# Kernel tuning notes

Hardware: AMD Instinct MI355X
Metric: run time of the kernel (lower is better)

The kernel has to match this reference:

```python
import jax, jax.numpy as jnp
import numpy as np

B, D, T = 32, 6, 2048
FH, ENC, H, CONF, NC, K = 128, 128, 256, 64, 10, 5


def setup_inputs() -> dict:
    key = jax.random.key(0)
    ks = iter(jax.random.split(key, 40))
    n = lambda shape, s=0.05: jax.random.normal(next(ks), shape, dtype=jnp.float32) * s
    inp = {
        'M': jax.random.normal(next(ks), (B, D, T), dtype=jnp.float32),
        # causal conv frontend (4 dilated convs, kernel 5)
        'conv_w0': n((FH, D, K)), 'conv_b0': n((FH,)),
        'conv_w1': n((FH, FH, K)), 'conv_b1': n((FH,)),
        'conv_w2': n((FH, FH, K)), 'conv_b2': n((FH,)),
        'conv_w3': n((FH, FH, K)), 'conv_b3': n((FH,)),
        # encoder projection
        'enc_w': n((ENC, FH)), 'enc_b': n((ENC,)),
        # selective state space
        'A': n((H, H), 0.01), 'ip_w': n((H, ENC)), 'ip_b': n((H,)),
        'state_bias': jnp.zeros((H,), jnp.float32),
        'op_w': n((H, H)), 'op_b': n((H,)),
        # classifier head
        'cls_w1': n((256, H)), 'cls_b1': n((256,)),
        'cls_w2': n((NC, 256)), 'cls_b2': n((NC,)),
        # metanet: 2*D -> 64 -> 128 -> confound_dim
        'mn_w1': n((64, 2 * D)), 'mn_b1': n((64,)),
        'mn_w2': n((128, 64)), 'mn_b2': n((128,)),
        'mn_w3': n((CONF, 128)), 'mn_b3': n((CONF,)),
        # frontdoor: confound_dim -> 128 -> ssm_hidden
        'fd_w1': n((128, CONF)), 'fd_b1': n((128,)),
        'fd_w2': n((H, 128)), 'fd_b2': n((H,)),
    }
    return inp


def _causal_conv(x, w, b, d):
    # x: (B,C,T), w: (O,I,K). pad-left (K-1)*d == pad-both + trim-right in torch code
    y = jax.lax.conv_general_dilated(
        x, w, window_strides=(1,), padding=[((w.shape[2] - 1) * d, 0)],
        rhs_dilation=(d,), dimension_numbers=('NCH', 'OIH', 'NCH'))
    return jax.nn.relu(y + b[None, :, None])


def reference(M, conv_w0, conv_b0, conv_w1, conv_b1, conv_w2, conv_b2, conv_w3, conv_b3,
              enc_w, enc_b, A, ip_w, ip_b, state_bias, op_w, op_b,
              cls_w1, cls_b1, cls_w2, cls_b2,
              mn_w1, mn_b1, mn_w2, mn_b2, mn_w3, mn_b3,
              fd_w1, fd_b1, fd_w2, fd_b2):
    # frontend: 4 causal dilated convs with ReLU
    out = M
    for w, b, d in ((conv_w0, conv_b0, 1), (conv_w1, conv_b1, 2),
                    (conv_w2, conv_b2, 4), (conv_w3, conv_b3, 8)):
        out = _causal_conv(out, w, b, d)
    feat = jnp.einsum('bct,ec->bte', out, enc_w) + enc_b  # (B,T,ENC)
    # SSM: precompute input projection, then sequential scan over T
    u = jnp.einsum('bte,he->bth', feat, ip_w) + ip_b + state_bias  # (B,T,H)

    def step(h, ut):
        h = jax.nn.gelu(h @ A.T + ut, approximate=False)
        return h, h

    h0 = jnp.zeros((M.shape[0], A.shape[0]), M.dtype)
    _, hs = jax.lax.scan(step, h0, jnp.swapaxes(u, 0, 1))  # hs: (T,B,H)
    ssm_out = jnp.einsum('tbh,gh->btg', hs, op_w) + op_b  # (B,T,H)
    pooled = ssm_out.mean(axis=1)  # (B,H)
    logits = jax.nn.relu(pooled @ cls_w1.T + cls_b1) @ cls_w2.T + cls_b2
    # confounder summary: mean & unbiased std over time
    s = jnp.concatenate([M.mean(axis=2), jnp.std(M, axis=2, ddof=1)], axis=1)
    z = jax.nn.relu(s @ mn_w1.T + mn_b1)
    z = jax.nn.relu(z @ mn_w2.T + mn_b2)
    conf_hat = z @ mn_w3.T + mn_b3
    adj = jax.nn.relu(conf_hat @ fd_w1.T + fd_b1) @ fd_w2.T + fd_b2
    corrected = pooled - adj
    return (logits, pooled, corrected, conf_hat)
```

## Files before the change

### kernel.cpp

```cpp
#include <hip/hip_runtime.h>
#include <cmath>


typedef __bf16 bf16_t;
typedef bf16_t bf16x8 __attribute__((ext_vector_type(8)));
typedef float f32x4 __attribute__((ext_vector_type(4)));

__device__ __forceinline__ f32x4 mfma16(bf16x8 a, bf16x8 b, f32x4 c) {
  return __builtin_amdgcn_mfma_f32_16x16x32_bf16(a, b, c, 0, 0, 0);
}

__device__ __forceinline__ float gelu_f(float x) {
  float a = x * 0.70710678118654752440f;
  float z = fabsf(a);
  float t = __builtin_amdgcn_rcpf(1.0f + 0.3275911f * z);
  float p = t * (0.254829592f +
            t * (-0.284496736f +
            t * (1.421413741f +
            t * (-1.453152027f +
            t * 1.061405429f))));
  float e = __expf(-z * z);
  float erf_a = __builtin_copysignf(1.0f - p * e, a);
  return 0.5f * x * (1.0f + erf_a);
}

__global__ void k_repack(const float* __restrict__ w0, const float* __restrict__ w1,
                         const float* __restrict__ w2, const float* __restrict__ w3,
                         bf16_t* __restrict__ wb0, bf16_t* __restrict__ wb1,
                         bf16_t* __restrict__ wb2, bf16_t* __restrict__ wb3) {
  int idx = blockIdx.x * 256 + threadIdx.x;
  if (idx < 128 * 32) {
    int o = idx >> 5, k = idx & 31;
    float v = 0.f;
    if (k < 30) { int i = k / 5, kk = k - i * 5; v = w0[(o * 6 + i) * 5 + kk]; }
    wb0[idx] = (bf16_t)v;
    return;
  }
  int e = idx - 128 * 32;
  if (e < 3 * 5 * 128 * 128) {
    int layer = e / (5 * 128 * 128);
    int r = e - layer * (5 * 128 * 128);
    int ks = r / 16384;
    int o = (r >> 7) & 127;
    int i = r & 127;
    const float* w = layer == 0 ? w1 : layer == 1 ? w2 : w3;
    bf16_t* wb = layer == 0 ? wb1 : layer == 1 ? wb2 : wb3;
    wb[r] = (bf16_t)w[(o * 128 + i) * 5 + ks];
  }
}

__global__ void k_wce(const float* __restrict__ ip_w, const float* __restrict__ enc_w,
                      const float* __restrict__ enc_b, const float* __restrict__ ip_b,
                      const float* __restrict__ sbias, bf16_t* __restrict__ wce,
                      float* __restrict__ bce) {
  int h = blockIdx.x, c = threadIdx.x;
  float s = 0.f;
  for (int e = 0; e < 128; ++e) s += ip_w[h * 128 + e] * enc_w[e * 128 + c];
  wce[h * 128 + c] = (bf16_t)s;
  if (c == 0) {
    float bv = 0.f;
    for (int e = 0; e < 128; ++e) bv += ip_w[h * 128 + e] * enc_b[e];
    bce[h] = bv + ip_b[h] + sbias[h];
  }
}

__global__ __launch_bounds__(256) void k_conv0(const float* __restrict__ M,
                                               const bf16_t* __restrict__ wb0,
                                               const float* __restrict__ b0,
                                               bf16_t* __restrict__ out) {
  __shared__ float raw[6][136];
  __shared__ bf16_t Xe[128 * 40];
  const int tid = threadIdx.x;
  const int b = blockIdx.y, t0 = blockIdx.x * 128;
  for (int id = tid; id < 6 * 132; id += 256) {
    int i = id / 132, j = id - i * 132;
    int t = t0 - 4 + j;
    raw[i][j] = (t >= 0) ? M[((size_t)b * 6 + i) * 2048 + t] : 0.f;
  }
  __syncthreads();
  for (int id = tid; id < 128 * 32; id += 256) {
    int tl = id >> 5, k = id & 31;
    float v = 0.f;
    if (k < 30) { int i = k / 5, kk = k - i * 5; v = raw[i][tl + kk]; }
    Xe[tl * 40 + k] = (bf16_t)v;
  }
  __syncthreads();
  const int w = tid >> 6, lane = tid & 63, q = lane >> 4, l15 = lane & 15;
  const int k0 = q * 8;
  const f32x4 z4 = {0.f, 0.f, 0.f, 0.f};
  f32x4 acc[2][8];
#pragma unroll
  for (int mt = 0; mt < 2; ++mt)
#pragma unroll
    for (int nt = 0; nt < 8; ++nt) acc[mt][nt] = z4;
  bf16x8 af[2];
#pragma unroll
  for (int mt = 0; mt < 2; ++mt)
    af[mt] = *(const bf16x8*)&Xe[(w * 32 + mt * 16 + l15) * 40 + k0];
#pragma unroll
  for (int nt = 0; nt < 8; ++nt) {
    bf16x8 bf = *(const bf16x8*)&wb0[(nt * 16 + l15) * 32 + k0];
#pragma unroll
    for (int mt = 0; mt < 2; ++mt) acc[mt][nt] = mfma16(af[mt], bf, acc[mt][nt]);
  }
#pragma unroll
  for (int nt = 0; nt < 8; ++nt) {
    const int o = nt * 16 + l15;
    const float bias = b0[o];
#pragma unroll
    for (int mt = 0; mt < 2; ++mt) {
#pragma unroll
      for (int r = 0; r < 4; ++r) {
        int t = t0 + w * 32 + mt * 16 + q * 4 + r;
        float v = acc[mt][nt][r] + bias;
        out[((size_t)b * 2048 + t) * 128 + o] = (bf16_t)(v > 0.f ? v : 0.f);
      }
    }
  }
}

template <int DIL>
__global__ __launch_bounds__(256) void k_conv(const bf16_t* __restrict__ in,
                                              const bf16_t* __restrict__ wb,
                                              const float* __restrict__ bias,
                                              bf16_t* __restrict__ out) {
  __shared__ bf16_t Xs[160 * 136];
  const int tid = threadIdx.x;
  const int b = blockIdx.y, t0 = blockIdx.x * 128;
  const bf16_t* src = in + (size_t)b * 2048 * 128;
  for (int id = tid; id < 160 * 16; id += 256) {
    int r = id >> 4, ck = id & 15;
    int t = t0 + r - 32;
    int4 v = make_int4(0, 0, 0, 0);
    if (t >= 0) v = *(const int4*)(src + (size_t)t * 128 + ck * 8);
    *(int4*)&Xs[r * 136 + ck * 8] = v;
  }
  __syncthreads();
  const int w = tid >> 6, lane = tid & 63, q = lane >> 4, l15 = lane & 15;
  const f32x4 z4 = {0.f, 0.f, 0.f, 0.f};
  f32x4 acc[2][8];
#pragma unroll
  for (int mt = 0; mt < 2; ++mt)
#pragma unroll
    for (int nt = 0; nt < 8; ++nt) acc[mt][nt] = z4;
#pragma unroll
  for (int ks = 0; ks < 5; ++ks) {
    const int shift = (4 - ks) * DIL;
#pragma unroll
    for (int kt = 0; kt < 4; ++kt) {
      const int k0 = kt * 32 + q * 8;
      bf16x8 af[2];
#pragma unroll
      for (int mt = 0; mt < 2; ++mt)
        af[mt] = *(const bf16x8*)&Xs[(32 + w * 32 + mt * 16 + l15 - shift) * 136 + k0];
#pragma unroll
      for (int nt = 0; nt < 8; ++nt) {
        bf16x8 bf = *(const bf16x8*)&wb[((size_t)ks * 128 + nt * 16 + l15) * 128 + k0];
#pragma unroll
        for (int mt = 0; mt < 2; ++mt) acc[mt][nt] = mfma16(af[mt], bf, acc[mt][nt]);
      }
    }
  }
#pragma unroll
  for (int nt = 0; nt < 8; ++nt) {
    const int o = nt * 16 + l15;
    const float bv = bias[o];
#pragma unroll
    for (int mt = 0; mt < 2; ++mt) {
#pragma unroll
      for (int r = 0; r < 4; ++r) {
        int t = t0 + w * 32 + mt * 16 + q * 4 + r;
        float v = acc[mt][nt][r] + bv;
        out[((size_t)b * 2048 + t) * 128 + o] = (bf16_t)(v > 0.f ? v : 0.f);
      }
    }
  }
}

__global__ __launch_bounds__(256) void k_ugemm(const bf16_t* __restrict__ in,
                                               const bf16_t* __restrict__ wce,
                                               const float* __restrict__ bce,
                                               bf16_t* __restrict__ u) {
  __shared__ bf16_t Xs[128 * 136];
  const int tid = threadIdx.x;
  const int b = blockIdx.y, t0 = blockIdx.x * 128, hh = blockIdx.z;
  const bf16_t* src = in + (size_t)b * 2048 * 128;
  for (int id = tid; id < 128 * 16; id += 256) {
    int r = id >> 4, ck = id & 15;
    *(int4*)&Xs[r * 136 + ck * 8] = *(const int4*)(src + (size_t)(t0 + r) * 128 + ck * 8);
  }
  __syncthreads();
  const int w = tid >> 6, lane = tid & 63, q = lane >> 4, l15 = lane & 15;
  const f32x4 z4 = {0.f, 0.f, 0.f, 0.f};
  f32x4 acc[2][8];
#pragma unroll
  for (int mt = 0; mt < 2; ++mt)
#pragma unroll
    for (int nt = 0; nt < 8; ++nt) acc[mt][nt] = z4;
#pragma unroll
  for (int kt = 0; kt < 4; ++kt) {
    const int k0 = kt * 32 + q * 8;
    bf16x8 af[2];
#pragma unroll
    for (int mt = 0; mt < 2; ++mt)
      af[mt] = *(const bf16x8*)&Xs[(w * 32 + mt * 16 + l15) * 136 + k0];
#pragma unroll
    for (int nt = 0; nt < 8; ++nt) {
      bf16x8 bf = *(const bf16x8*)&wce[((size_t)hh * 128 + nt * 16 + l15) * 128 + k0];
#pragma unroll
      for (int mt = 0; mt < 2; ++mt) acc[mt][nt] = mfma16(af[mt], bf, acc[mt][nt]);
    }
  }
#pragma unroll
  for (int nt = 0; nt < 8; ++nt) {
    const int h = hh * 128 + nt * 16 + l15;
    const float bv = bce[h];
#pragma unroll
    for (int mt = 0; mt < 2; ++mt) {
#pragma unroll
      for (int r = 0; r < 4; ++r) {
        int t = t0 + w * 32 + mt * 16 + q * 4 + r;
        u[((size_t)b * 2048 + t) * 256 + h] = (bf16_t)(acc[mt][nt][r] + bv);
      }
    }
  }
}

__global__ __launch_bounds__(256, 1) void k_scan(const float* __restrict__ Am,
                                                 const bf16_t* __restrict__ u,
                                                 float* __restrict__ hbarOut) {
  __shared__ bf16_t hb[2][256];
  const int b = blockIdx.x;
  const int tid = threadIdx.x;
  const int w = tid >> 6, lane = tid & 63, q = lane >> 4, l15 = lane & 15;

  bf16x8 bfr[4][8];
#pragma unroll
  for (int nt = 0; nt < 4; ++nt) {
    const int c = w * 64 + nt * 16 + l15;
#pragma unroll
    for (int kt = 0; kt < 8; ++kt) {
      const float* ap = Am + (size_t)c * 256 + kt * 32 + q * 8;
      f32x4 p0 = *(const f32x4*)ap;
      f32x4 p1 = *(const f32x4*)(ap + 4);
      bf16x8 v;
      v[0] = (bf16_t)p0[0]; v[1] = (bf16_t)p0[1]; v[2] = (bf16_t)p0[2]; v[3] = (bf16_t)p0[3];
      v[4] = (bf16_t)p1[0]; v[5] = (bf16_t)p1[1]; v[6] = (bf16_t)p1[2]; v[7] = (bf16_t)p1[3];
      bfr[nt][kt] = v;
    }
  }
  hb[0][tid] = (bf16_t)0.f;
  hb[1][tid] = (bf16_t)0.f;
  const bf16_t* up = u + (size_t)b * 2048 * 256 + tid;
  float hbar = 0.f;
  bf16_t ua = up[0];
  bf16_t ub = up[256];
  __syncthreads();

  const f32x4 z4 = {0.f, 0.f, 0.f, 0.f};

#define SCAN_STEP(RD, WR, UREG)                                   \
  {                                                               \
    f32x4 acc[4] = {z4, z4, z4, z4};                              \
    _Pragma("unroll")                                             \
    for (int kt = 0; kt < 8; ++kt) {                              \
      bf16x8 af = *(const bf16x8*)&hb[RD][kt * 32 + q * 8];       \
      _Pragma("unroll")                                           \
      for (int nt = 0; nt < 4; ++nt)                              \
        acc[nt] = mfma16(af, bfr[nt][kt], acc[nt]);               \
    }                                                             \
    float y = (q == 0) ? acc[0][0] : (q == 1) ? acc[1][0]         \
            : (q == 2) ? acc[2][0] : acc[3][0];                   \
    float g = gelu_f(y + (float)(UREG));                          \
    hbar += g;                                                    \
    hb[WR][tid] = (bf16_t)g;                                      \
    asm volatile("s_waitcnt lgkmcnt(0)" ::: "memory");            \
    __builtin_amdgcn_s_barrier();                                 \
    __builtin_amdgcn_sched_barrier(0);                            \
  }

  for (int t = 0; t < 2048; t += 2) {
    bf16_t ua2 = (t + 2 < 2048) ? up[(size_t)(t + 2) * 256] : (bf16_t)0.f;
    SCAN_STEP(0, 1, ua)
    bf16_t ub2 = (t + 3 < 2048) ? up[(size_t)(t + 3) * 256] : (bf16_t)0.f;
    SCAN_STEP(1, 0, ub)
    ua = ua2;
    ub = ub2;
  }
#undef SCAN_STEP

  hbarOut[b * 256 + tid] = hbar * (1.f / 2048.f);
}

__global__ void k_meta1(const float* __restrict__ M, float* __restrict__ stats) {
  const int c = blockIdx.x, b = blockIdx.y, tid = threadIdx.x;
  const float* p = M + ((size_t)b * 6 + c) * 2048;
  float s = 0.f, ss = 0.f;
  for (int t = tid; t < 2048; t += 256) { float v = p[t]; s += v; ss += v * v; }
  for (int o = 32; o > 0; o >>= 1) { s += __shfl_down(s, o, 64); ss += __shfl_down(ss, o, 64); }
  __shared__ float as_[4], ass_[4];
  const int w = tid >> 6, lane = tid & 63;
  if (lane == 0) { as_[w] = s; ass_[w] = ss; }
  __syncthreads();
  if (tid == 0) {
    s = as_[0] + as_[1] + as_[2] + as_[3];
    ss = ass_[0] + ass_[1] + ass_[2] + ass_[3];
    float mean = s * (1.f / 2048.f);
    float var = (ss - 2048.f * mean * mean) * (1.f / 2047.f);
    if (var < 0.f) var = 0.f;
    stats[b * 12 + c] = mean;
    stats[b * 12 + 6 + c] = sqrtf(var);
  }
}

__global__ void k_meta2(const float* __restrict__ stats,
                        const float* __restrict__ w1, const float* __restrict__ b1,
                        const float* __restrict__ w2, const float* __restrict__ b2,
                        const float* __restrict__ w3, const float* __restrict__ b3,
                        const float* __restrict__ f1, const float* __restrict__ fb1,
                        const float* __restrict__ f2, const float* __restrict__ fb2,
                        float* __restrict__ out, float* __restrict__ adj) {
  const int b = blockIdx.x, tid = threadIdx.x;
  __shared__ float s[12], z1[64], z2[128], ch[64], a1[128];
  if (tid < 12) s[tid] = stats[b * 12 + tid];
  __syncthreads();
  if (tid < 64) {
    float v = b1[tid];
    for (int e = 0; e < 12; ++e) v += w1[tid * 12 + e] * s[e];
    z1[tid] = v > 0.f ? v : 0.f;
  }
  __syncthreads();
  if (tid < 128) {
    float v = b2[tid];
    for (int e = 0; e < 64; ++e) v += w2[tid * 64 + e] * z1[e];
    z2[tid] = v > 0.f ? v : 0.f;
  }
  __syncthreads();
  if (tid < 64) {
    float v = b3[tid];
    for (int e = 0; e < 128; ++e) v += w3[tid * 128 + e] * z2[e];
    ch[tid] = v;
    out[16704 + b * 64 + tid] = v;
  }
  __syncthreads();
  if (tid < 128) {
    float v = fb1[tid];
    for (int e = 0; e < 64; ++e) v += f1[tid * 64 + e] * ch[e];
    a1[tid] = v > 0.f ? v : 0.f;
  }
  __syncthreads();
  {
    float v = fb2[tid];
    for (int e = 0; e < 128; ++e) v += f2[tid * 128 + e] * a1[e];
    adj[b * 256 + tid] = v;
  }
}

__global__ void k_head(const float* __restrict__ hbar, const float* __restrict__ op_w,
                       const float* __restrict__ op_b, const float* __restrict__ cw1,
                       const float* __restrict__ cb1, const float* __restrict__ cw2,
                       const float* __restrict__ cb2, const float* __restrict__ adj,
                       float* __restrict__ out) {
  const int b = blockIdx.x, g = threadIdx.x;
  __shared__ float hs[256], ps[256], hid[256];
  hs[g] = hbar[b * 256 + g];
  __syncthreads();
  float v = op_b[g];
  for (int h = 0; h < 256; ++h) v += op_w[g * 256 + h] * hs[h];
  out[320 + b * 256 + g] = v;
  out[8512 + b * 256 + g] = v - adj[b * 256 + g];
  ps[g] = v;
  __syncthreads();
  float hv = cb1[g];
  for (int h = 0; h < 256; ++h) hv += cw1[g * 256 + h] * ps[h];
  hid[g] = hv > 0.f ? hv : 0.f;
  __syncthreads();
  if (g < 10) {
    float lv = cb2[g];
    for (int h = 0; h < 256; ++h) lv += cw2[g * 256 + h] * hid[h];
    out[b * 10 + g] = lv;
  }
}

extern "C" void kernel_launch(void* const* d_in, const int* in_sizes, int n_in,
                              void* d_out, int out_size, void* d_ws, size_t ws_size,
                              hipStream_t stream) {
  (void)in_sizes; (void)n_in; (void)out_size; (void)ws_size;
  const float* M    = (const float*)d_in[0];
  const float* w0   = (const float*)d_in[1];  const float* b0  = (const float*)d_in[2];
  const float* w1   = (const float*)d_in[3];  const float* b1  = (const float*)d_in[4];
  const float* w2   = (const float*)d_in[5];  const float* b2  = (const float*)d_in[6];
  const float* w3   = (const float*)d_in[7];  const float* b3  = (const float*)d_in[8];
  const float* encw = (const float*)d_in[9];  const float* encb = (const float*)d_in[10];
  const float* Am   = (const float*)d_in[11];
  const float* ipw  = (const float*)d_in[12]; const float* ipb = (const float*)d_in[13];
  const float* sb   = (const float*)d_in[14];
  const float* opw  = (const float*)d_in[15]; const float* opb = (const float*)d_in[16];
  const float* cw1  = (const float*)d_in[17]; const float* cb1 = (const float*)d_in[18];
  const float* cw2  = (const float*)d_in[19]; const float* cb2 = (const float*)d_in[20];
  const float* mw1  = (const float*)d_in[21]; const float* mb1 = (const float*)d_in[22];
  const float* mw2  = (const float*)d_in[23]; const float* mb2 = (const float*)d_in[24];
  const float* mw3  = (const float*)d_in[25]; const float* mb3 = (const float*)d_in[26];
  const float* fw1  = (const float*)d_in[27]; const float* fb1 = (const float*)d_in[28];
  const float* fw2  = (const float*)d_in[29]; const float* fb2 = (const float*)d_in[30];
  float* out = (float*)d_out;

  char* ws = (char*)d_ws;
  bf16_t* wb0  = (bf16_t*)(ws + 0);
  bf16_t* wb1  = (bf16_t*)(ws + 8192);
  bf16_t* wb2  = (bf16_t*)(ws + 172032);
  bf16_t* wb3  = (bf16_t*)(ws + 335872);
  bf16_t* wce  = (bf16_t*)(ws + 499712);
  float*  bce  = (float*) (ws + 565248);
  float*  hbar = (float*) (ws + 566272);
  float*  adj  = (float*) (ws + 599040);
  float*  stats= (float*) (ws + 631808);
  bf16_t* actA = (bf16_t*)(ws + 633856);
  bf16_t* actB = (bf16_t*)(ws + 17411072);
  bf16_t* u    = (bf16_t*)(ws + 34188288);

  k_repack<<<976, 256, 0, stream>>>(w0, w1, w2, w3, wb0, wb1, wb2, wb3);
  k_wce<<<256, 128, 0, stream>>>(ipw, encw, encb, ipb, sb, wce, bce);
  k_conv0<<<dim3(16, 32), 256, 0, stream>>>(M, wb0, b0, actA);
  k_conv<2><<<dim3(16, 32), 256, 0, stream>>>(actA, wb1, b1, actB);
  k_conv<4><<<dim3(16, 32), 256, 0, stream>>>(actB, wb2, b2, actA);
  k_conv<8><<<dim3(16, 32), 256, 0, stream>>>(actA, wb3, b3, actB);
  k_ugemm<<<dim3(16, 32, 2), 256, 0, stream>>>(actB, wce, bce, u);
  k_scan<<<32, 256, 0, stream>>>(Am, u, hbar);
  k_meta1<<<dim3(6, 32), 256, 0, stream>>>(M, stats);
  k_meta2<<<32, 256, 0, stream>>>(stats, mw1, mb1, mw2, mb2, mw3, mb3,
                                  fw1, fb1, fw2, fb2, out, adj);
  k_head<<<32, 256, 0, stream>>>(hbar, opw, opb, cw1, cb1, cw2, cb2, adj, out);
}
```

Before: 1.422 ms.

## Fuse prep and post kernels, fold input into scan MFMA accumulator

Merges the weight repack and the encoder/input-projection fold into one prep launch, and merges the stats, metanet and head kernels into one post launch, cutting the launch count. In the scan step, all A-fragments are loaded up front, the input u is seeded into the MFMA accumulator instead of being added afterwards, and sched_group_barrier hints order the LDS reads before the MFMAs. The hbar accumulation moves after the barrier so it is off the critical path. The fused post kernel computes the statistics serially over 6 channels in 32 blocks, which lowers parallelism for that part.

```diff
diff --git a/kernel.cpp b/kernel.cpp
--- a/kernel.cpp
+++ b/kernel.cpp
@@ -24,11 +24,29 @@
   return 0.5f * x * (1.0f + erf_a);
 }
 
-__global__ void k_repack(const float* __restrict__ w0, const float* __restrict__ w1,
-                         const float* __restrict__ w2, const float* __restrict__ w3,
-                         bf16_t* __restrict__ wb0, bf16_t* __restrict__ wb1,
-                         bf16_t* __restrict__ wb2, bf16_t* __restrict__ wb3) {
-  int idx = blockIdx.x * 256 + threadIdx.x;
+__global__ void k_prep(const float* __restrict__ w0, const float* __restrict__ w1,
+                       const float* __restrict__ w2, const float* __restrict__ w3,
+                       const float* __restrict__ ip_w, const float* __restrict__ enc_w,
+                       const float* __restrict__ enc_b, const float* __restrict__ ip_b,
+                       const float* __restrict__ sbias,
+                       bf16_t* __restrict__ wb0, bf16_t* __restrict__ wb1,
+                       bf16_t* __restrict__ wb2, bf16_t* __restrict__ wb3,
+                       bf16_t* __restrict__ wce, float* __restrict__ bce) {
+  int bid = blockIdx.x;
+  if (bid >= 976) {
+    int idx = (bid - 976) * 256 + threadIdx.x;
+    int h = idx >> 7, c = idx & 127;
+    float s = 0.f;
+    for (int e = 0; e < 128; ++e) s += ip_w[h * 128 + e] * enc_w[e * 128 + c];
+    wce[h * 128 + c] = (bf16_t)s;
+    if (c == 0) {
+      float bv = 0.f;
+      for (int e = 0; e < 128; ++e) bv += ip_w[h * 128 + e] * enc_b[e];
+      bce[h] = bv + ip_b[h] + sbias[h];
+    }
+    return;
+  }
+  int idx = bid * 256 + threadIdx.x;
   if (idx < 128 * 32) {
     int o = idx >> 5, k = idx & 31;
     float v = 0.f;
@@ -46,21 +64,6 @@
     const float* w = layer == 0 ? w1 : layer == 1 ? w2 : w3;
     bf16_t* wb = layer == 0 ? wb1 : layer == 1 ? wb2 : wb3;
     wb[r] = (bf16_t)w[(o * 128 + i) * 5 + ks];
-  }
-}
-
-__global__ void k_wce(const float* __restrict__ ip_w, const float* __restrict__ enc_w,
-                      const float* __restrict__ enc_b, const float* __restrict__ ip_b,
-                      const float* __restrict__ sbias, bf16_t* __restrict__ wce,
-                      float* __restrict__ bce) {
-  int h = blockIdx.x, c = threadIdx.x;
-  float s = 0.f;
-  for (int e = 0; e < 128; ++e) s += ip_w[h * 128 + e] * enc_w[e * 128 + c];
-  wce[h * 128 + c] = (bf16_t)s;
-  if (c == 0) {
-    float bv = 0.f;
-    for (int e = 0; e < 128; ++e) bv += ip_w[h * 128 + e] * enc_b[e];
-    bce[h] = bv + ip_b[h] + sbias[h];
   }
 }
 
@@ -261,22 +264,33 @@
 
 #define SCAN_STEP(RD, WR, UREG)                                   \
   {                                                               \
-    f32x4 acc[4] = {z4, z4, z4, z4};                              \
+    bf16x8 af[8];                                                 \
+    _Pragma("unroll")                                             \
+    for (int kt = 0; kt < 8; ++kt)                                \
+      af[kt] = *(const bf16x8*)&hb[RD][kt * 32 + q * 8];          \
+    float uin = (float)(UREG);                                    \
+    f32x4 acc[4];                                                 \
+    _Pragma("unroll")                                             \
+    for (int nt = 0; nt < 4; ++nt) {                              \
+      acc[nt] = z4;                                               \
+      acc[nt][0] = (q == nt) ? uin : 0.f;                         \
+    }                                                             \
     _Pragma("unroll")                                             \
     for (int kt = 0; kt < 8; ++kt) {                              \
-      bf16x8 af = *(const bf16x8*)&hb[RD][kt * 32 + q * 8];       \
       _Pragma("unroll")                                           \
       for (int nt = 0; nt < 4; ++nt)                              \
-        acc[nt] = mfma16(af, bfr[nt][kt], acc[nt]);               \
+        acc[nt] = mfma16(af[kt], bfr[nt][kt], acc[nt]);           \
     }                                                             \
+    __builtin_amdgcn_sched_group_barrier(0x100, 8, 0);            \
+    __builtin_amdgcn_sched_group_barrier(0x008, 32, 0);           \
     float y = (q == 0) ? acc[0][0] : (q == 1) ? acc[1][0]         \
             : (q == 2) ? acc[2][0] : acc[3][0];                   \
-    float g = gelu_f(y + (float)(UREG));                          \
-    hbar += g;                                                    \
+    float g = gelu_f(y);                                          \
     hb[WR][tid] = (bf16_t)g;                                      \
     asm volatile("s_waitcnt lgkmcnt(0)" ::: "memory");            \
     __builtin_amdgcn_s_barrier();                                 \
     __builtin_amdgcn_sched_barrier(0);                            \
+    hbar += g;                                                    \
   }
 
   for (int t = 0; t < 2048; t += 2) {
@@ -292,41 +306,43 @@
   hbarOut[b * 256 + tid] = hbar * (1.f / 2048.f);
 }
 
-__global__ void k_meta1(const float* __restrict__ M, float* __restrict__ stats) {
-  const int c = blockIdx.x, b = blockIdx.y, tid = threadIdx.x;
-  const float* p = M + ((size_t)b * 6 + c) * 2048;
-  float s = 0.f, ss = 0.f;
-  for (int t = tid; t < 2048; t += 256) { float v = p[t]; s += v; ss += v * v; }
-  for (int o = 32; o > 0; o >>= 1) { s += __shfl_down(s, o, 64); ss += __shfl_down(ss, o, 64); }
+__global__ __launch_bounds__(256) void k_post(
+    const float* __restrict__ M, const float* __restrict__ hbar,
+    const float* __restrict__ w1, const float* __restrict__ b1,
+    const float* __restrict__ w2, const float* __restrict__ b2,
+    const float* __restrict__ w3, const float* __restrict__ b3,
+    const float* __restrict__ f1, const float* __restrict__ fb1,
+    const float* __restrict__ f2, const float* __restrict__ fb2,
+    const float* __restrict__ op_w, const float* __restrict__ op_b,
+    const float* __restrict__ cw1, const float* __restrict__ cb1,
+    const float* __restrict__ cw2, const float* __restrict__ cb2,
+    float* __restrict__ out) {
+  const int b = blockIdx.x, tid = threadIdx.x;
+  const int w = tid >> 6, lane = tid & 63;
+  __shared__ float s12[12], z1[64], z2[128], ch[64], a1[128], adjs[256];
+  __shared__ float hs[256], ps[256], hid[256];
   __shared__ float as_[4], ass_[4];
-  const int w = tid >> 6, lane = tid & 63;
-  if (lane == 0) { as_[w] = s; ass_[w] = ss; }
-  __syncthreads();
-  if (tid == 0) {
-    s = as_[0] + as_[1] + as_[2] + as_[3];
-    ss = ass_[0] + ass_[1] + ass_[2] + ass_[3];
-    float mean = s * (1.f / 2048.f);
-    float var = (ss - 2048.f * mean * mean) * (1.f / 2047.f);
-    if (var < 0.f) var = 0.f;
-    stats[b * 12 + c] = mean;
-    stats[b * 12 + 6 + c] = sqrtf(var);
-  }
-}
-
-__global__ void k_meta2(const float* __restrict__ stats,
-                        const float* __restrict__ w1, const float* __restrict__ b1,
-                        const float* __restrict__ w2, const float* __restrict__ b2,
-                        const float* __restrict__ w3, const float* __restrict__ b3,
-                        const float* __restrict__ f1, const float* __restrict__ fb1,
-                        const float* __restrict__ f2, const float* __restrict__ fb2,
-                        float* __restrict__ out, float* __restrict__ adj) {
-  const int b = blockIdx.x, tid = threadIdx.x;
-  __shared__ float s[12], z1[64], z2[128], ch[64], a1[128];
-  if (tid < 12) s[tid] = stats[b * 12 + tid];
-  __syncthreads();
+  for (int c = 0; c < 6; ++c) {
+    const float* p = M + ((size_t)b * 6 + c) * 2048;
+    float s = 0.f, ss = 0.f;
+    for (int t = tid; t < 2048; t += 256) { float v = p[t]; s += v; ss += v * v; }
+    for (int o = 32; o > 0; o >>= 1) { s += __shfl_down(s, o, 64); ss += __shfl_down(ss, o, 64); }
+    if (lane == 0) { as_[w] = s; ass_[w] = ss; }
+    __syncthreads();
+    if (tid == 0) {
+      s = as_[0] + as_[1] + as_[2] + as_[3];
+      ss = ass_[0] + ass_[1] + ass_[2] + ass_[3];
+      float mean = s * (1.f / 2048.f);
+      float var = (ss - 2048.f * mean * mean) * (1.f / 2047.f);
+      if (var < 0.f) var = 0.f;
+      s12[c] = mean;
+      s12[6 + c] = sqrtf(var);
+    }
+    __syncthreads();
+  }
   if (tid < 64) {
     float v = b1[tid];
-    for (int e = 0; e < 12; ++e) v += w1[tid * 12 + e] * s[e];
+    for (int e = 0; e < 12; ++e) v += w1[tid * 12 + e] * s12[e];
     z1[tid] = v > 0.f ? v : 0.f;
   }
   __syncthreads();
@@ -352,33 +368,24 @@
   {
     float v = fb2[tid];
     for (int e = 0; e < 128; ++e) v += f2[tid * 128 + e] * a1[e];
-    adj[b * 256 + tid] = v;
-  }
-}
-
-__global__ void k_head(const float* __restrict__ hbar, const float* __restrict__ op_w,
-                       const float* __restrict__ op_b, const float* __restrict__ cw1,
-                       const float* __restrict__ cb1, const float* __restrict__ cw2,
-                       const float* __restrict__ cb2, const float* __restrict__ adj,
-                       float* __restrict__ out) {
-  const int b = blockIdx.x, g = threadIdx.x;
-  __shared__ float hs[256], ps[256], hid[256];
-  hs[g] = hbar[b * 256 + g];
-  __syncthreads();
-  float v = op_b[g];
-  for (int h = 0; h < 256; ++h) v += op_w[g * 256 + h] * hs[h];
-  out[320 + b * 256 + g] = v;
-  out[8512 + b * 256 + g] = v - adj[b * 256 + g];
-  ps[g] = v;
-  __syncthreads();
-  float hv = cb1[g];
-  for (int h = 0; h < 256; ++h) hv += cw1[g * 256 + h] * ps[h];
-  hid[g] = hv > 0.f ? hv : 0.f;
-  __syncthreads();
-  if (g < 10) {
-    float lv = cb2[g];
-    for (int h = 0; h < 256; ++h) lv += cw2[g * 256 + h] * hid[h];
-    out[b * 10 + g] = lv;
+    adjs[tid] = v;
+  }
+  hs[tid] = hbar[b * 256 + tid];
+  __syncthreads();
+  float v = op_b[tid];
+  for (int h = 0; h < 256; ++h) v += op_w[tid * 256 + h] * hs[h];
+  out[320 + b * 256 + tid] = v;
+  out[8512 + b * 256 + tid] = v - adjs[tid];
+  ps[tid] = v;
+  __syncthreads();
+  float hv = cb1[tid];
+  for (int h = 0; h < 256; ++h) hv += cw1[tid * 256 + h] * ps[h];
+  hid[tid] = hv > 0.f ? hv : 0.f;
+  __syncthreads();
+  if (tid < 10) {
+    float lv = cb2[tid];
+    for (int h = 0; h < 256; ++h) lv += cw2[tid * 256 + h] * hid[h];
+    out[b * 10 + tid] = lv;
   }
 }
 
@@ -413,22 +420,19 @@
   bf16_t* wce  = (bf16_t*)(ws + 499712);
   float*  bce  = (float*) (ws + 565248);
   float*  hbar = (float*) (ws + 566272);
-  float*  adj  = (float*) (ws + 599040);
-  float*  stats= (float*) (ws + 631808);
   bf16_t* actA = (bf16_t*)(ws + 633856);
   bf16_t* actB = (bf16_t*)(ws + 17411072);
   bf16_t* u    = (bf16_t*)(ws + 34188288);
 
-  k_repack<<<976, 256, 0, stream>>>(w0, w1, w2, w3, wb0, wb1, wb2, wb3);
-  k_wce<<<256, 128, 0, stream>>>(ipw, encw, encb, ipb, sb, wce, bce);
+  k_prep<<<1104, 256, 0, stream>>>(w0, w1, w2, w3, ipw, encw, encb, ipb, sb,
+                                   wb0, wb1, wb2, wb3, wce, bce);
   k_conv0<<<dim3(16, 32), 256, 0, stream>>>(M, wb0, b0, actA);
   k_conv<2><<<dim3(16, 32), 256, 0, stream>>>(actA, wb1, b1, actB);
   k_conv<4><<<dim3(16, 32), 256, 0, stream>>>(actB, wb2, b2, actA);
   k_conv<8><<<dim3(16, 32), 256, 0, stream>>>(actA, wb3, b3, actB);
   k_ugemm<<<dim3(16, 32, 2), 256, 0, stream>>>(actB, wce, bce, u);
   k_scan<<<32, 256, 0, stream>>>(Am, u, hbar);
-  k_meta1<<<dim3(6, 32), 256, 0, stream>>>(M, stats);
-  k_meta2<<<32, 256, 0, stream>>>(stats, mw1, mb1, mw2, mb2, mw3, mb3,
-                                  fw1, fb1, fw2, fb2, out, adj);
-  k_head<<<32, 256, 0, stream>>>(hbar, opw, opb, cw1, cb1, cw2, cb2, adj, out);
-}
+  k_post<<<32, 256, 0, stream>>>(M, hbar, mw1, mb1, mw2, mb2, mw3, mb3,
+                                 fw1, fb1, fw2, fb2, opw, opb,
+                                 cw1, cb1, cw2, cb2, out);
+}
```

New measurement: 1.407 ms (median of 3 runs). About the same (-1.1%).
